# Kernel optimization log

Measured on AMD Instinct MI355X. Metric: run time of the kernel, lower is better.

## Reference

```python
import jax, jax.numpy as jnp
import numpy as np
import math

SEQ_LEN = 32768
DIM = 64
HYPER = [2048, 1024, 512]
POOL = [2, 2]
K = 16
UPDATE_RATE = 0.5
ALPHA = 3.0


def _node_nums():
    n = [SEQ_LEN]
    for p in POOL:
        n.append(n[-1] // p)
    return n[:len(HYPER)]  # [32768, 16384, 8192]


def _init_adj(n, h, k):
    # Faithful port of init_H_indicies for one level: banded 0/1 matrix, then softmax over dim=1
    m = np.zeros((n, h), dtype=np.float32)
    for col in range(h - 1, -1, -1):
        s = max(0, n - k - h + col - 1)
        e = n - h + col
        if s <= e:
            m[s:e + 1, col] = 1.0
    x = m - m.max(axis=1, keepdims=True)
    ex = np.exp(x)
    return (ex / ex.sum(axis=1, keepdims=True)).astype(np.float32)


def setup_inputs() -> dict:
    key = jax.random.key(0)
    ks = jax.random.split(key, 6)
    nn_ = _node_nums()
    inp = {}
    for i, n in enumerate(nn_):
        inp[f"node_emb{i}"] = jax.random.normal(ks[i], (n, DIM), dtype=jnp.float32)
    for i, h in enumerate(HYPER):
        inp[f"edge_emb{i}"] = jax.random.normal(ks[3 + i], (h, DIM), dtype=jnp.float32)
    for i, (n, h) in enumerate(zip(nn_, HYPER)):
        inp[f"adj_init{i}"] = jnp.asarray(_init_adj(n, h, K))
    return inp


def _layer(node, edge, adj_prev):
    # a = node @ edge.T ; cur = softmax(relu(alpha*a), dim=1)
    a = jnp.matmul(node, edge.T)  # [N, E]
    cur = jax.nn.softmax(jax.nn.relu(ALPHA * a), axis=1)
    k = min(cur.shape[1], K)
    _, idx = jax.lax.top_k(cur, k)  # [N, k]
    rows = jnp.arange(cur.shape[0])[:, None]
    mask = jnp.zeros_like(cur).at[rows, idx].set(1.0)  # scatter_ with s1.fill_(1)
    cur = cur * mask
    adj = UPDATE_RATE * cur + (1.0 - UPDATE_RATE) * adj_prev  # EMA blend
    adj = (adj - adj.min()) / (adj.max() - adj.min())  # global minmax norm
    return adj


def _binarize(adj):
    b = (adj > 0.5)
    retain = b.any(axis=0)  # which hyperedges survive compaction (H2index retain_edge)
    return b.astype(jnp.int32), retain


def reference(node_emb0, node_emb1, node_emb2, edge_emb0, edge_emb1, edge_emb2,
              adj_init0, adj_init1, adj_init2):
    nodes = [node_emb0, node_emb1, node_emb2]
    edges = [edge_emb0, edge_emb1, edge_emb2]
    inits = [adj_init0, adj_init1, adj_init2]
    H_list, bins, retains = [], [], []
    for nd, ed, ad in zip(nodes, edges, inits):
        adj = _layer(nd, ed, ad)
        H_list.append(adj)
        b, r = _binarize(adj)
        bins.append(b)
        retains.append(r)
    # Hypergraph fusion (HypergraphFusion is not defined in the source; we use the
    # natural fusion: upsample each coarse level to seq_len resolution by repeating
    # each coarse node over its pooling window, then concat along the hyperedge axis).
    full = []
    factor = 1
    for i, H in enumerate(H_list):
        up = jnp.repeat(H, factor, axis=0)  # [node_num[i]*factor, E_i] == [SEQ_LEN, E_i]
        if up.shape[0] < SEQ_LEN:
            up = jnp.pad(up, ((0, SEQ_LEN - up.shape[0]), (0, 0)))
        full.append(up)
        if i < len(POOL):
            factor *= POOL[i]
    fused_H = jnp.concatenate(full, axis=1)  # [SEQ_LEN, sum(HYPER)]
    fused_bin, fused_retain = _binarize(fused_H)
    return (fused_H, H_list[0], H_list[1], H_list[2],
            bins[0], bins[1], bins[2], fused_bin,
            retains[0], retains[1], retains[2], fused_retain)
```

## Files before the change

### kernel.cpp

```cpp
#include <hip/hip_runtime.h>
#include <cstdint>
#include <cstddef>

#define DIM 64

static constexpr size_t OFF_FH = 0;
static constexpr size_t OFF_H0 = 117440512;
static constexpr size_t OFF_H1 = 184549376;
static constexpr size_t OFF_H2 = 201326592;
static constexpr size_t OFF_B0 = 205520896;
static constexpr size_t OFF_B1 = 272629760;
static constexpr size_t OFF_B2 = 289406976;
static constexpr size_t OFF_FB = 293601280;
static constexpr size_t OFF_R0 = 411041792;
static constexpr size_t OFF_R1 = 411043840;
static constexpr size_t OFF_R2 = 411044864;
static constexpr size_t OFF_RF = 411045376;

__device__ __forceinline__ double exp2split(float x) {
  const float f = x * 1.44269504f;
  const int i = (int)f;
  const float r = f - (float)i;
  const float e = exp2f(r);
  const unsigned long long sc = (unsigned long long)(1023 + i) << 52;
  return (double)e * __longlong_as_double((long long)sc);
}

__device__ __forceinline__ void scan1(float x, int col, unsigned long long* top,
                                      unsigned long long& tmin, double& s) {
  const unsigned long long pk =
      ((unsigned long long)__float_as_uint(x) << 32) |
      (unsigned long long)(0xFFFFFFFFu - (unsigned int)col);
  if (pk > tmin) {
#pragma unroll
    for (int q = 0; q < 16; ++q) top[q] = (top[q] == tmin) ? pk : top[q];
    unsigned long long t2 = top[0];
#pragma unroll
    for (int q = 1; q < 16; ++q) t2 = (top[q] < t2) ? top[q] : t2;
    tmin = t2;
  }
  s += exp2split(x);
}

__global__ void k_init(float* __restrict__ out, unsigned int* __restrict__ wsMM,
                       unsigned long long* __restrict__ wsBlend) {
  const int t = threadIdx.x;
  for (int i = t; i < 7168; i += 256) out[OFF_R0 + i] = 0.0f;
  if (t < 3) {
    wsMM[2 * t + 0] = 0x7F7FFFFFu;
    wsMM[2 * t + 1] = 0u;
    wsBlend[t] = 0ull;
  }
}

__global__ __launch_bounds__(256) void k1(
    const float* __restrict__ node0, const float* __restrict__ node1, const float* __restrict__ node2,
    const float* __restrict__ edge0, const float* __restrict__ edge1, const float* __restrict__ edge2,
    const float* __restrict__ init0, const float* __restrict__ init1, const float* __restrict__ init2,
    int* __restrict__ tIdx0, int* __restrict__ tIdx1, int* __restrict__ tIdx2,
    double* __restrict__ tCur0, double* __restrict__ tCur1, double* __restrict__ tCur2,
    unsigned int* __restrict__ wsMM, unsigned long long* __restrict__ wsBlend) {
  __shared__ float smem[128 * 132];
  __shared__ float sMin[4], sMax[4];
  __shared__ double sBlendW[4];

  const int b = blockIdx.x;
  int lvl, bloc, E;
  const float *node, *edge, *init;
  int* tIdx;
  double* tCur;
  if (b < 256)      { lvl = 0; bloc = b;       node = node0; edge = edge0; init = init0; tIdx = tIdx0; tCur = tCur0; E = 2048; }
  else if (b < 384) { lvl = 1; bloc = b - 256; node = node1; edge = edge1; init = init1; tIdx = tIdx1; tCur = tCur1; E = 1024; }
  else              { lvl = 2; bloc = b - 384; node = node2; edge = edge2; init = init2; tIdx = tIdx2; tCur = tCur2; E = 512;  }

  const int t = threadIdx.x;
  const int lane = t & 63;
  const int wave = t >> 6;
  const int row0 = bloc * 128;
  const int tr8 = (t & 15) << 3;
  const int tc8 = (t >> 4) << 3;
  const int srow = t >> 1;
  const int sl = t & 1;
  float* nB = smem + 64 * 132;

  unsigned long long top[16];
#pragma unroll
  for (int q = 0; q < 16; ++q) top[q] = (unsigned long long)q;
  unsigned long long tmin = 0ull;
  double s0 = 0.0, s1 = 0.0;

  for (int c0 = 0; c0 < E; c0 += 128) {
    __syncthreads();
#pragma unroll
    for (int p = 0; p < 8; ++p) {
      const int idx = t + 256 * p;
      const int r = idx >> 4;
      const int kc = (idx & 15) << 2;
      const float4 v = *(const float4*)(node + (size_t)(row0 + r) * DIM + kc);
      smem[(kc + 0) * 132 + r] = v.x;
      smem[(kc + 1) * 132 + r] = v.y;
      smem[(kc + 2) * 132 + r] = v.z;
      smem[(kc + 3) * 132 + r] = v.w;
      const float4 w = *(const float4*)(edge + (size_t)(c0 + r) * DIM + kc);
      nB[(kc + 0) * 132 + r] = w.x;
      nB[(kc + 1) * 132 + r] = w.y;
      nB[(kc + 2) * 132 + r] = w.z;
      nB[(kc + 3) * 132 + r] = w.w;
    }
    __syncthreads();

    float acc[8][8];
#pragma unroll
    for (int i = 0; i < 8; ++i)
#pragma unroll
      for (int j = 0; j < 8; ++j) acc[i][j] = 0.0f;

#pragma unroll 4
    for (int k = 0; k < 64; ++k) {
      const float4 a0 = *(const float4*)&smem[k * 132 + tr8];
      const float4 a1 = *(const float4*)&smem[k * 132 + tr8 + 4];
      const float4 b0 = *(const float4*)&nB[k * 132 + tc8];
      const float4 b1 = *(const float4*)&nB[k * 132 + tc8 + 4];
      const float av[8] = {a0.x, a0.y, a0.z, a0.w, a1.x, a1.y, a1.z, a1.w};
      const float bv[8] = {b0.x, b0.y, b0.z, b0.w, b1.x, b1.y, b1.z, b1.w};
#pragma unroll
      for (int i = 0; i < 8; ++i)
#pragma unroll
        for (int j = 0; j < 8; ++j) acc[i][j] = fmaf(av[i], bv[j], acc[i][j]);
    }
    __syncthreads();

#pragma unroll
    for (int i = 0; i < 8; ++i) {
      float4 h0, h1;
      h0.x = fmaxf(3.0f * acc[i][0], 0.0f); h0.y = fmaxf(3.0f * acc[i][1], 0.0f);
      h0.z = fmaxf(3.0f * acc[i][2], 0.0f); h0.w = fmaxf(3.0f * acc[i][3], 0.0f);
      h1.x = fmaxf(3.0f * acc[i][4], 0.0f); h1.y = fmaxf(3.0f * acc[i][5], 0.0f);
      h1.z = fmaxf(3.0f * acc[i][6], 0.0f); h1.w = fmaxf(3.0f * acc[i][7], 0.0f);
      *(float4*)&smem[(tr8 + i) * 132 + tc8] = h0;
      *(float4*)&smem[(tr8 + i) * 132 + tc8 + 4] = h1;
    }
    __syncthreads();

#pragma unroll 4
    for (int j = 0; j < 16; ++j) {
      const int cl = (sl << 6) + (j << 2);
      const float4 v = *(const float4*)&smem[srow * 132 + cl];
      const int cb = c0 + cl;
      scan1(v.x, cb + 0, top, tmin, s0);
      scan1(v.y, cb + 1, top, tmin, s1);
      scan1(v.z, cb + 2, top, tmin, s0);
      scan1(v.w, cb + 3, top, tmin, s1);
    }
  }

  unsigned long long win[8];
#pragma unroll 1
  for (int round = 0; round < 16; ++round) {
    unsigned long long lm = top[0];
#pragma unroll
    for (int q = 1; q < 16; ++q) lm = (top[q] > lm) ? top[q] : lm;
    { const unsigned long long o = __shfl_xor(lm, 1); lm = (o > lm) ? o : lm; }
#pragma unroll
    for (int q = 0; q < 16; ++q) top[q] = (top[q] == lm) ? 0ull : top[q];
    if ((round & 1) == sl) win[round >> 1] = lm;
  }

  double sAll = s0 + s1;
  sAll += __shfl_xor(sAll, 1);

  const int grow = row0 + srow;
  const float4* n4 = (const float4*)(node + (size_t)grow * DIM);
  double eh[8];
  int gcv[8];
  double h32sum = 0.0, ehsum = 0.0;
#pragma unroll 1
  for (int w = 0; w < 8; ++w) {
    const float x32 = __uint_as_float((unsigned int)(win[w] >> 32));
    const unsigned int gc = 0xFFFFFFFFu - (unsigned int)(win[w] & 0xFFFFFFFFull);
    const float4* e4 = (const float4*)(edge + (size_t)gc * DIM);
    double acc = 0.0;
#pragma unroll
    for (int j = 0; j < 16; ++j) {
      const float4 a = n4[j], bb = e4[j];
      acc += (double)a.x * (double)bb.x + (double)a.y * (double)bb.y +
             (double)a.z * (double)bb.z + (double)a.w * (double)bb.w;
    }
    const double x64 = fmax(3.0 * acc, 0.0);
    eh[w] = exp(x64);
    ehsum += eh[w];
    h32sum += exp2split(x32);
    gcv[w] = (int)gc;
  }
  h32sum += __shfl_xor(h32sum, 1);
  ehsum += __shfl_xor(ehsum, 1);
  const double sFix = fmax(sAll - h32sum, 0.0) + ehsum;

  double blend = 0.0;
#pragma unroll 1
  for (int w = 0; w < 8; ++w) {
    const double cur = eh[w] / sFix;
    tIdx[(size_t)grow * 16 + 2 * w + sl] = gcv[w];
    tCur[(size_t)grow * 16 + 2 * w + sl] = cur;
    blend = fmax(blend, 0.5 * ((double)init[(size_t)grow * E + gcv[w]] + cur));
  }
#pragma unroll
  for (int d = 1; d < 64; d <<= 1) {
    const double o = __shfl_xor(blend, d);
    blend = fmax(blend, o);
  }
  if (lane == 0) sBlendW[wave] = blend;

  float imn = __uint_as_float(0x7F7FFFFFu), imx = 0.0f;
  const float4* ib = (const float4*)(init + (size_t)row0 * E);
  const int tot = (128 * E) >> 2;
  for (int i = t; i < tot; i += 256) {
    const float4 v = ib[i];
    imn = fminf(imn, fminf(fminf(v.x, v.y), fminf(v.z, v.w)));
    imx = fmaxf(imx, fmaxf(fmaxf(v.x, v.y), fmaxf(v.z, v.w)));
  }
#pragma unroll
  for (int d = 1; d < 64; d <<= 1) {
    imn = fminf(imn, __shfl_xor(imn, d));
    imx = fmaxf(imx, __shfl_xor(imx, d));
  }
  if (lane == 0) { sMin[wave] = imn; sMax[wave] = imx; }
  __syncthreads();
  if (t == 0) {
    const float a = fminf(fminf(sMin[0], sMin[1]), fminf(sMin[2], sMin[3]));
    const float bmx = fmaxf(fmaxf(sMax[0], sMax[1]), fmaxf(sMax[2], sMax[3]));
    atomicMin(wsMM + 2 * lvl + 0, __float_as_uint(a));
    atomicMax(wsMM + 2 * lvl + 1, __float_as_uint(bmx));
    double bl = sBlendW[0];
#pragma unroll
    for (int i = 1; i < 4; ++i) bl = fmax(bl, sBlendW[i]);
    atomicMax(wsBlend + lvl, (unsigned long long)__double_as_longlong(bl));
  }
}

__global__ __launch_bounds__(256) void k2(
    const float* __restrict__ init0, const float* __restrict__ init1, const float* __restrict__ init2,
    const int* __restrict__ tIdx0, const int* __restrict__ tIdx1, const int* __restrict__ tIdx2,
    const double* __restrict__ tCur0, const double* __restrict__ tCur1, const double* __restrict__ tCur2,
    const unsigned int* __restrict__ wsMM, const unsigned long long* __restrict__ wsBlend,
    float* __restrict__ out) {
  __shared__ float fH[3584];
  __shared__ float fB[3584];
  const int r = blockIdx.x;
  const int t = threadIdx.x;
  const int r1 = r >> 1, r2 = r >> 2;

  const double mn0 = 0.5 * (double)__uint_as_float(wsMM[0]);
  const double mx0 = fmax(0.5 * (double)__uint_as_float(wsMM[1]),
                          __longlong_as_double((long long)wsBlend[0]));
  const double inv0 = 1.0 / (mx0 - mn0);
  const double mn1 = 0.5 * (double)__uint_as_float(wsMM[2]);
  const double mx1 = fmax(0.5 * (double)__uint_as_float(wsMM[3]),
                          __longlong_as_double((long long)wsBlend[1]));
  const double inv1 = 1.0 / (mx1 - mn1);
  const double mn2 = 0.5 * (double)__uint_as_float(wsMM[4]);
  const double mx2 = fmax(0.5 * (double)__uint_as_float(wsMM[5]),
                          __longlong_as_double((long long)wsBlend[2]));
  const double inv2 = 1.0 / (mx2 - mn2);

  for (int i = t; i < 896; i += 256) {
    const int c = i << 2;
    float4 v;
    float mnl, il;
    size_t offR, offF;
    if (c < 2048)      { v = *(const float4*)(init0 + (size_t)r  * 2048 + c);
                         mnl = (float)mn0; il = (float)inv0; offR = OFF_R0; offF = (size_t)c; }
    else if (c < 3072) { v = *(const float4*)(init1 + (size_t)r1 * 1024 + (c - 2048));
                         mnl = (float)mn1; il = (float)inv1; offR = OFF_R1 - 2048; offF = (size_t)c; }
    else               { v = *(const float4*)(init2 + (size_t)r2 * 512 + (c - 3072));
                         mnl = (float)mn2; il = (float)inv2; offR = OFF_R2 - 3072; offF = (size_t)c; }
    float4 h, bb;
    h.x = (0.5f * v.x - mnl) * il;
    h.y = (0.5f * v.y - mnl) * il;
    h.z = (0.5f * v.z - mnl) * il;
    h.w = (0.5f * v.w - mnl) * il;
    bb.x = (h.x > 0.5f) ? 1.0f : 0.0f;
    bb.y = (h.y > 0.5f) ? 1.0f : 0.0f;
    bb.z = (h.z > 0.5f) ? 1.0f : 0.0f;
    bb.w = (h.w > 0.5f) ? 1.0f : 0.0f;
    *(float4*)&fH[c] = h;
    *(float4*)&fB[c] = bb;
    if (bb.x + bb.y + bb.z + bb.w > 0.0f) {
      if (bb.x > 0.0f) { out[offR + c + 0] = 1.0f; out[OFF_RF + c + 0] = 1.0f; }
      if (bb.y > 0.0f) { out[offR + c + 1] = 1.0f; out[OFF_RF + c + 1] = 1.0f; }
      if (bb.z > 0.0f) { out[offR + c + 2] = 1.0f; out[OFF_RF + c + 2] = 1.0f; }
      if (bb.w > 0.0f) { out[offR + c + 3] = 1.0f; out[OFF_RF + c + 3] = 1.0f; }
    }
  }
  __syncthreads();

  if (t < 48) {
    const int lv = t >> 4, j = t & 15;
    int rowl, El, off;
    const int* ti; const double* tc; const float* in;
    size_t offR;
    double mnl, il;
    if (lv == 0)      { rowl = r;  El = 2048; off = 0;    ti = tIdx0; tc = tCur0; in = init0; offR = OFF_R0; mnl = mn0; il = inv0; }
    else if (lv == 1) { rowl = r1; El = 1024; off = 2048; ti = tIdx1; tc = tCur1; in = init1; offR = OFF_R1; mnl = mn1; il = inv1; }
    else              { rowl = r2; El = 512;  off = 3072; ti = tIdx2; tc = tCur2; in = init2; offR = OFF_R2; mnl = mn2; il = inv2; }
    const int gc = ti[(size_t)rowl * 16 + j];
    const double cur = tc[(size_t)rowl * 16 + j];
    const double adj = 0.5 * ((double)in[(size_t)rowl * El + gc] + cur);
    const double H = (adj - mnl) * il;
    const float hf = (float)H;
    const float bf = (H > 0.5) ? 1.0f : 0.0f;
    fH[off + gc] = hf;
    fB[off + gc] = bf;
    if (bf > 0.0f) {
      out[offR + gc] = 1.0f;
      out[OFF_RF + off + gc] = 1.0f;
    }
  }
  __syncthreads();

  const float4* sH = (const float4*)fH;
  const float4* sB = (const float4*)fB;
  float4* FH = (float4*)(out + OFF_FH + (size_t)r * 3584);
  float4* FB = (float4*)(out + OFF_FB + (size_t)r * 3584);
  float4* H0 = (float4*)(out + OFF_H0 + (size_t)r * 2048);
  float4* B0 = (float4*)(out + OFF_B0 + (size_t)r * 2048);
  for (int i = t; i < 896; i += 256) { FH[i] = sH[i]; FB[i] = sB[i]; }
  for (int i = t; i < 512; i += 256) { H0[i] = sH[i]; B0[i] = sB[i]; }
  if ((r & 1) == 0) {
    float4* H1 = (float4*)(out + OFF_H1 + (size_t)r1 * 1024);
    float4* B1 = (float4*)(out + OFF_B1 + (size_t)r1 * 1024);
    H1[t] = sH[512 + t];
    B1[t] = sB[512 + t];
  }
  if ((r & 3) == 0 && t < 128) {
    float4* H2 = (float4*)(out + OFF_H2 + (size_t)r2 * 512);
    float4* B2 = (float4*)(out + OFF_B2 + (size_t)r2 * 512);
    H2[t] = sH[768 + t];
    B2[t] = sB[768 + t];
  }
}

extern "C" void kernel_launch(void* const* d_in, const int* in_sizes, int n_in,
                              void* d_out, int out_size, void* d_ws, size_t ws_size,
                              hipStream_t stream) {
  (void)in_sizes; (void)n_in; (void)out_size; (void)ws_size;
  const float* node0 = (const float*)d_in[0];
  const float* node1 = (const float*)d_in[1];
  const float* node2 = (const float*)d_in[2];
  const float* edge0 = (const float*)d_in[3];
  const float* edge1 = (const float*)d_in[4];
  const float* edge2 = (const float*)d_in[5];
  const float* init0 = (const float*)d_in[6];
  const float* init1 = (const float*)d_in[7];
  const float* init2 = (const float*)d_in[8];
  float* out = (float*)d_out;

  unsigned char* ws = (unsigned char*)d_ws;
  unsigned int* wsMM = (unsigned int*)ws;
  unsigned long long* wsBlend = (unsigned long long*)(ws + 32);
  int*    tIdx0 = (int*)(ws + 64);
  int*    tIdx1 = (int*)(ws + 64 + (size_t)(2 << 20));
  int*    tIdx2 = (int*)(ws + 64 + (size_t)(3 << 20));
  double* tCur0 = (double*)(ws + 64 + (size_t)(4 << 20));
  double* tCur1 = (double*)(ws + 64 + (size_t)(8 << 20));
  double* tCur2 = (double*)(ws + 64 + (size_t)(10 << 20));

  k_init<<<1, 256, 0, stream>>>(out, wsMM, wsBlend);
  k1<<<448, 256, 0, stream>>>(node0, node1, node2, edge0, edge1, edge2,
                              init0, init1, init2, tIdx0, tIdx1, tIdx2,
                              tCur0, tCur1, tCur2, wsMM, wsBlend);
  k2<<<32768, 256, 0, stream>>>(init0, init1, init2, tIdx0, tIdx1, tIdx2,
                                tCur0, tCur1, tCur2, wsMM, wsBlend, out);
}
```

Measured before the change: 2.625 ms.

## Split fused GEMM/top-k kernel into GEMM, minmax and per-row wave top-k kernels

The monolithic k1, which ran only 448 blocks, is split in three. k1a computes relu(3*A·Eᵀ) tiles and writes them to a workspace buffer. A separate kmm kernel does the global min/max over the init matrices. k1b assigns one wavefront per row to scan the staged logits, select the top-16 with wave-wide shuffles, and do the fp64 refinement. The aim is to fix poor occupancy and parallelism in the serial per-thread top-k scan, at the cost of writing and re-reading about 450MB of intermediate logits. Nontemporal stores are also added for the k2 output writes.

```diff
diff --git a/kernel.cpp b/kernel.cpp
--- a/kernel.cpp
+++ b/kernel.cpp
@@ -3,6 +3,8 @@
 #include <cstddef>
 
 #define DIM 64
+
+typedef float f32x4 __attribute__((ext_vector_type(4)));
 
 static constexpr size_t OFF_FH = 0;
 static constexpr size_t OFF_H0 = 117440512;
@@ -53,59 +55,39 @@
   }
 }
 
-__global__ __launch_bounds__(256) void k1(
+__global__ __launch_bounds__(256, 2) void k1a(
     const float* __restrict__ node0, const float* __restrict__ node1, const float* __restrict__ node2,
     const float* __restrict__ edge0, const float* __restrict__ edge1, const float* __restrict__ edge2,
-    const float* __restrict__ init0, const float* __restrict__ init1, const float* __restrict__ init2,
-    int* __restrict__ tIdx0, int* __restrict__ tIdx1, int* __restrict__ tIdx2,
-    double* __restrict__ tCur0, double* __restrict__ tCur1, double* __restrict__ tCur2,
-    unsigned int* __restrict__ wsMM, unsigned long long* __restrict__ wsBlend) {
-  __shared__ float smem[128 * 132];
-  __shared__ float sMin[4], sMax[4];
-  __shared__ double sBlendW[4];
+    float* __restrict__ xt0, float* __restrict__ xt1, float* __restrict__ xt2) {
+  __shared__ float sA[64 * 132];
+  __shared__ float sB[64 * 132];
 
   const int b = blockIdx.x;
-  int lvl, bloc, E;
-  const float *node, *edge, *init;
-  int* tIdx;
-  double* tCur;
-  if (b < 256)      { lvl = 0; bloc = b;       node = node0; edge = edge0; init = init0; tIdx = tIdx0; tCur = tCur0; E = 2048; }
-  else if (b < 384) { lvl = 1; bloc = b - 256; node = node1; edge = edge1; init = init1; tIdx = tIdx1; tCur = tCur1; E = 1024; }
-  else              { lvl = 2; bloc = b - 384; node = node2; edge = edge2; init = init2; tIdx = tIdx2; tCur = tCur2; E = 512;  }
+  int bloc, E;
+  const float *node, *edge;
+  float* xt;
+  if (b < 256)      { bloc = b;       node = node0; edge = edge0; xt = xt0; E = 2048; }
+  else if (b < 384) { bloc = b - 256; node = node1; edge = edge1; xt = xt1; E = 1024; }
+  else              { bloc = b - 384; node = node2; edge = edge2; xt = xt2; E = 512;  }
 
   const int t = threadIdx.x;
-  const int lane = t & 63;
-  const int wave = t >> 6;
   const int row0 = bloc * 128;
-  const int tr8 = (t & 15) << 3;
-  const int tc8 = (t >> 4) << 3;
-  const int srow = t >> 1;
-  const int sl = t & 1;
-  float* nB = smem + 64 * 132;
-
-  unsigned long long top[16];
-#pragma unroll
-  for (int q = 0; q < 16; ++q) top[q] = (unsigned long long)q;
-  unsigned long long tmin = 0ull;
-  double s0 = 0.0, s1 = 0.0;
+  const int tr8 = (t >> 4) << 3;
+  const int tc8 = (t & 15) << 3;
 
   for (int c0 = 0; c0 < E; c0 += 128) {
     __syncthreads();
 #pragma unroll
     for (int p = 0; p < 8; ++p) {
-      const int idx = t + 256 * p;
-      const int r = idx >> 4;
-      const int kc = (idx & 15) << 2;
+      const int idx = t + (p << 8);
+      const int kc = (idx >> 7) << 2;
+      const int r = idx & 127;
       const float4 v = *(const float4*)(node + (size_t)(row0 + r) * DIM + kc);
-      smem[(kc + 0) * 132 + r] = v.x;
-      smem[(kc + 1) * 132 + r] = v.y;
-      smem[(kc + 2) * 132 + r] = v.z;
-      smem[(kc + 3) * 132 + r] = v.w;
+      sA[(kc + 0) * 132 + r] = v.x; sA[(kc + 1) * 132 + r] = v.y;
+      sA[(kc + 2) * 132 + r] = v.z; sA[(kc + 3) * 132 + r] = v.w;
       const float4 w = *(const float4*)(edge + (size_t)(c0 + r) * DIM + kc);
-      nB[(kc + 0) * 132 + r] = w.x;
-      nB[(kc + 1) * 132 + r] = w.y;
-      nB[(kc + 2) * 132 + r] = w.z;
-      nB[(kc + 3) * 132 + r] = w.w;
+      sB[(kc + 0) * 132 + r] = w.x; sB[(kc + 1) * 132 + r] = w.y;
+      sB[(kc + 2) * 132 + r] = w.z; sB[(kc + 3) * 132 + r] = w.w;
     }
     __syncthreads();
 
@@ -115,12 +97,12 @@
 #pragma unroll
       for (int j = 0; j < 8; ++j) acc[i][j] = 0.0f;
 
-#pragma unroll 4
+#pragma unroll 2
     for (int k = 0; k < 64; ++k) {
-      const float4 a0 = *(const float4*)&smem[k * 132 + tr8];
-      const float4 a1 = *(const float4*)&smem[k * 132 + tr8 + 4];
-      const float4 b0 = *(const float4*)&nB[k * 132 + tc8];
-      const float4 b1 = *(const float4*)&nB[k * 132 + tc8 + 4];
+      const float4 a0 = *(const float4*)&sA[k * 132 + tr8];
+      const float4 a1 = *(const float4*)&sA[k * 132 + tr8 + 4];
+      const float4 b0 = *(const float4*)&sB[k * 132 + tc8];
+      const float4 b1 = *(const float4*)&sB[k * 132 + tc8 + 4];
       const float av[8] = {a0.x, a0.y, a0.z, a0.w, a1.x, a1.y, a1.z, a1.w};
       const float bv[8] = {b0.x, b0.y, b0.z, b0.w, b1.x, b1.y, b1.z, b1.w};
 #pragma unroll
@@ -128,56 +110,119 @@
 #pragma unroll
         for (int j = 0; j < 8; ++j) acc[i][j] = fmaf(av[i], bv[j], acc[i][j]);
     }
-    __syncthreads();
 
 #pragma unroll
     for (int i = 0; i < 8; ++i) {
-      float4 h0, h1;
+      f32x4 h0, h1;
       h0.x = fmaxf(3.0f * acc[i][0], 0.0f); h0.y = fmaxf(3.0f * acc[i][1], 0.0f);
       h0.z = fmaxf(3.0f * acc[i][2], 0.0f); h0.w = fmaxf(3.0f * acc[i][3], 0.0f);
       h1.x = fmaxf(3.0f * acc[i][4], 0.0f); h1.y = fmaxf(3.0f * acc[i][5], 0.0f);
       h1.z = fmaxf(3.0f * acc[i][6], 0.0f); h1.w = fmaxf(3.0f * acc[i][7], 0.0f);
-      *(float4*)&smem[(tr8 + i) * 132 + tc8] = h0;
-      *(float4*)&smem[(tr8 + i) * 132 + tc8 + 4] = h1;
-    }
-    __syncthreads();
-
-#pragma unroll 4
-    for (int j = 0; j < 16; ++j) {
-      const int cl = (sl << 6) + (j << 2);
-      const float4 v = *(const float4*)&smem[srow * 132 + cl];
-      const int cb = c0 + cl;
-      scan1(v.x, cb + 0, top, tmin, s0);
-      scan1(v.y, cb + 1, top, tmin, s1);
-      scan1(v.z, cb + 2, top, tmin, s0);
-      scan1(v.w, cb + 3, top, tmin, s1);
-    }
-  }
-
-  unsigned long long win[8];
+      float* dst = xt + (size_t)(row0 + tr8 + i) * E + c0 + tc8;
+      *(f32x4*)dst = h0;
+      *(f32x4*)(dst + 4) = h1;
+    }
+  }
+}
+
+__global__ __launch_bounds__(256) void kmm(
+    const float* __restrict__ init0, const float* __restrict__ init1,
+    const float* __restrict__ init2, unsigned int* __restrict__ wsMM) {
+  __shared__ float sMin[3][4], sMax[3][4];
+  const int t = threadIdx.x;
+  const int lane = t & 63;
+  const int wave = t >> 6;
+  const int gid = blockIdx.x * 256 + t;
+  const int stride = gridDim.x * 256;
+  const float* inits[3] = {init0, init1, init2};
+  const int n4[3] = {16777216, 4194304, 1048576};
+#pragma unroll
+  for (int lv = 0; lv < 3; ++lv) {
+    float mn = __uint_as_float(0x7F7FFFFFu), mx = 0.0f;
+    const float4* p = (const float4*)inits[lv];
+    for (int i = gid; i < n4[lv]; i += stride) {
+      const float4 v = p[i];
+      mn = fminf(mn, fminf(fminf(v.x, v.y), fminf(v.z, v.w)));
+      mx = fmaxf(mx, fmaxf(fmaxf(v.x, v.y), fmaxf(v.z, v.w)));
+    }
+#pragma unroll
+    for (int d = 1; d < 64; d <<= 1) {
+      mn = fminf(mn, __shfl_xor(mn, d));
+      mx = fmaxf(mx, __shfl_xor(mx, d));
+    }
+    if (lane == 0) { sMin[lv][wave] = mn; sMax[lv][wave] = mx; }
+  }
+  __syncthreads();
+  if (t < 3) {
+    const float a = fminf(fminf(sMin[t][0], sMin[t][1]), fminf(sMin[t][2], sMin[t][3]));
+    const float b = fmaxf(fmaxf(sMax[t][0], sMax[t][1]), fmaxf(sMax[t][2], sMax[t][3]));
+    atomicMin(wsMM + 2 * t + 0, __float_as_uint(a));
+    atomicMax(wsMM + 2 * t + 1, __float_as_uint(b));
+  }
+}
+
+__global__ __launch_bounds__(256) void k1b(
+    const float* __restrict__ node0, const float* __restrict__ node1, const float* __restrict__ node2,
+    const float* __restrict__ edge0, const float* __restrict__ edge1, const float* __restrict__ edge2,
+    const float* __restrict__ init0, const float* __restrict__ init1, const float* __restrict__ init2,
+    const float* __restrict__ xt0, const float* __restrict__ xt1, const float* __restrict__ xt2,
+    int* __restrict__ tIdx0, int* __restrict__ tIdx1, int* __restrict__ tIdx2,
+    double* __restrict__ tCur0, double* __restrict__ tCur1, double* __restrict__ tCur2,
+    unsigned long long* __restrict__ wsBlend) {
+  __shared__ double sBlend[4];
+  const int t = threadIdx.x;
+  const int lane = t & 63;
+  const int gw = blockIdx.x * 4 + (t >> 6);
+  int lvl, row, E;
+  const float *xt, *node, *edge, *init;
+  int* tIdx;
+  double* tCur;
+  if (gw < 32768)      { lvl = 0; row = gw;          E = 2048; xt = xt0; node = node0; edge = edge0; init = init0; tIdx = tIdx0; tCur = tCur0; }
+  else if (gw < 49152) { lvl = 1; row = gw - 32768;  E = 1024; xt = xt1; node = node1; edge = edge1; init = init1; tIdx = tIdx1; tCur = tCur1; }
+  else                 { lvl = 2; row = gw - 49152;  E = 512;  xt = xt2; node = node2; edge = edge2; init = init2; tIdx = tIdx2; tCur = tCur2; }
+
+  const float* xrow = xt + (size_t)row * E;
+  unsigned long long top[16];
+#pragma unroll
+  for (int q = 0; q < 16; ++q) top[q] = (unsigned long long)q;
+  unsigned long long tmin = 0ull;
+  double s = 0.0;
+  const int nIt = E >> 8;
+  for (int j = 0; j < nIt; ++j) {
+    const int c4 = (lane + (j << 6)) << 2;
+    const float4 v = *(const float4*)(xrow + c4);
+    scan1(v.x, c4 + 0, top, tmin, s);
+    scan1(v.y, c4 + 1, top, tmin, s);
+    scan1(v.z, c4 + 2, top, tmin, s);
+    scan1(v.w, c4 + 3, top, tmin, s);
+  }
+
+  unsigned long long mywin = 0ull;
 #pragma unroll 1
   for (int round = 0; round < 16; ++round) {
     unsigned long long lm = top[0];
 #pragma unroll
     for (int q = 1; q < 16; ++q) lm = (top[q] > lm) ? top[q] : lm;
-    { const unsigned long long o = __shfl_xor(lm, 1); lm = (o > lm) ? o : lm; }
+#pragma unroll
+    for (int d = 1; d < 64; d <<= 1) {
+      const unsigned long long o = __shfl_xor(lm, d);
+      lm = (o > lm) ? o : lm;
+    }
 #pragma unroll
     for (int q = 0; q < 16; ++q) top[q] = (top[q] == lm) ? 0ull : top[q];
-    if ((round & 1) == sl) win[round >> 1] = lm;
-  }
-
-  double sAll = s0 + s1;
-  sAll += __shfl_xor(sAll, 1);
-
-  const int grow = row0 + srow;
-  const float4* n4 = (const float4*)(node + (size_t)grow * DIM);
-  double eh[8];
-  int gcv[8];
-  double h32sum = 0.0, ehsum = 0.0;
-#pragma unroll 1
-  for (int w = 0; w < 8; ++w) {
-    const float x32 = __uint_as_float((unsigned int)(win[w] >> 32));
-    const unsigned int gc = 0xFFFFFFFFu - (unsigned int)(win[w] & 0xFFFFFFFFull);
+    if (lane == round) mywin = lm;
+  }
+
+  double sAll = s;
+#pragma unroll
+  for (int d = 1; d < 64; d <<= 1) sAll += __shfl_xor(sAll, d);
+
+  double eh = 0.0, h32 = 0.0;
+  int gc = 0;
+  if (lane < 16) {
+    const float x32 = __uint_as_float((unsigned int)(mywin >> 32));
+    gc = (int)(0xFFFFFFFFu - (unsigned int)(mywin & 0xFFFFFFFFull));
+    const float4* n4 = (const float4*)(node + (size_t)row * DIM);
     const float4* e4 = (const float4*)(edge + (size_t)gc * DIM);
     double acc = 0.0;
 #pragma unroll
@@ -186,54 +231,35 @@
       acc += (double)a.x * (double)bb.x + (double)a.y * (double)bb.y +
              (double)a.z * (double)bb.z + (double)a.w * (double)bb.w;
     }
-    const double x64 = fmax(3.0 * acc, 0.0);
-    eh[w] = exp(x64);
-    ehsum += eh[w];
-    h32sum += exp2split(x32);
-    gcv[w] = (int)gc;
-  }
-  h32sum += __shfl_xor(h32sum, 1);
-  ehsum += __shfl_xor(ehsum, 1);
+    eh = exp(fmax(3.0 * acc, 0.0));
+    h32 = exp2split(x32);
+  }
+  double ehsum = eh, h32sum = h32;
+#pragma unroll
+  for (int d = 1; d < 64; d <<= 1) {
+    ehsum += __shfl_xor(ehsum, d);
+    h32sum += __shfl_xor(h32sum, d);
+  }
   const double sFix = fmax(sAll - h32sum, 0.0) + ehsum;
 
   double blend = 0.0;
-#pragma unroll 1
-  for (int w = 0; w < 8; ++w) {
-    const double cur = eh[w] / sFix;
-    tIdx[(size_t)grow * 16 + 2 * w + sl] = gcv[w];
-    tCur[(size_t)grow * 16 + 2 * w + sl] = cur;
-    blend = fmax(blend, 0.5 * ((double)init[(size_t)grow * E + gcv[w]] + cur));
+  if (lane < 16) {
+    const double cur = eh / sFix;
+    tIdx[(size_t)row * 16 + lane] = gc;
+    tCur[(size_t)row * 16 + lane] = cur;
+    blend = 0.5 * ((double)init[(size_t)row * E + gc] + cur);
   }
 #pragma unroll
   for (int d = 1; d < 64; d <<= 1) {
     const double o = __shfl_xor(blend, d);
     blend = fmax(blend, o);
   }
-  if (lane == 0) sBlendW[wave] = blend;
-
-  float imn = __uint_as_float(0x7F7FFFFFu), imx = 0.0f;
-  const float4* ib = (const float4*)(init + (size_t)row0 * E);
-  const int tot = (128 * E) >> 2;
-  for (int i = t; i < tot; i += 256) {
-    const float4 v = ib[i];
-    imn = fminf(imn, fminf(fminf(v.x, v.y), fminf(v.z, v.w)));
-    imx = fmaxf(imx, fmaxf(fmaxf(v.x, v.y), fmaxf(v.z, v.w)));
-  }
-#pragma unroll
-  for (int d = 1; d < 64; d <<= 1) {
-    imn = fminf(imn, __shfl_xor(imn, d));
-    imx = fmaxf(imx, __shfl_xor(imx, d));
-  }
-  if (lane == 0) { sMin[wave] = imn; sMax[wave] = imx; }
+  if (lane == 0) sBlend[t >> 6] = blend;
   __syncthreads();
   if (t == 0) {
-    const float a = fminf(fminf(sMin[0], sMin[1]), fminf(sMin[2], sMin[3]));
-    const float bmx = fmaxf(fmaxf(sMax[0], sMax[1]), fmaxf(sMax[2], sMax[3]));
-    atomicMin(wsMM + 2 * lvl + 0, __float_as_uint(a));
-    atomicMax(wsMM + 2 * lvl + 1, __float_as_uint(bmx));
-    double bl = sBlendW[0];
-#pragma unroll
-    for (int i = 1; i < 4; ++i) bl = fmax(bl, sBlendW[i]);
+    double bl = sBlend[0];
+#pragma unroll
+    for (int i = 1; i < 4; ++i) bl = fmax(bl, sBlend[i]);
     atomicMax(wsBlend + lvl, (unsigned long long)__double_as_longlong(bl));
   }
 }
@@ -267,13 +293,13 @@
     const int c = i << 2;
     float4 v;
     float mnl, il;
-    size_t offR, offF;
+    size_t offR;
     if (c < 2048)      { v = *(const float4*)(init0 + (size_t)r  * 2048 + c);
-                         mnl = (float)mn0; il = (float)inv0; offR = OFF_R0; offF = (size_t)c; }
+                         mnl = (float)mn0; il = (float)inv0; offR = OFF_R0; }
     else if (c < 3072) { v = *(const float4*)(init1 + (size_t)r1 * 1024 + (c - 2048));
-                         mnl = (float)mn1; il = (float)inv1; offR = OFF_R1 - 2048; offF = (size_t)c; }
+                         mnl = (float)mn1; il = (float)inv1; offR = OFF_R1 - 2048; }
     else               { v = *(const float4*)(init2 + (size_t)r2 * 512 + (c - 3072));
-                         mnl = (float)mn2; il = (float)inv2; offR = OFF_R2 - 3072; offF = (size_t)c; }
+                         mnl = (float)mn2; il = (float)inv2; offR = OFF_R2 - 3072; }
     float4 h, bb;
     h.x = (0.5f * v.x - mnl) * il;
     h.y = (0.5f * v.y - mnl) * il;
@@ -318,25 +344,31 @@
   }
   __syncthreads();
 
-  const float4* sH = (const float4*)fH;
-  const float4* sB = (const float4*)fB;
-  float4* FH = (float4*)(out + OFF_FH + (size_t)r * 3584);
-  float4* FB = (float4*)(out + OFF_FB + (size_t)r * 3584);
-  float4* H0 = (float4*)(out + OFF_H0 + (size_t)r * 2048);
-  float4* B0 = (float4*)(out + OFF_B0 + (size_t)r * 2048);
-  for (int i = t; i < 896; i += 256) { FH[i] = sH[i]; FB[i] = sB[i]; }
-  for (int i = t; i < 512; i += 256) { H0[i] = sH[i]; B0[i] = sB[i]; }
+  const f32x4* sH = (const f32x4*)fH;
+  const f32x4* sB = (const f32x4*)fB;
+  f32x4* FH = (f32x4*)(out + OFF_FH + (size_t)r * 3584);
+  f32x4* FB = (f32x4*)(out + OFF_FB + (size_t)r * 3584);
+  f32x4* H0 = (f32x4*)(out + OFF_H0 + (size_t)r * 2048);
+  f32x4* B0 = (f32x4*)(out + OFF_B0 + (size_t)r * 2048);
+  for (int i = t; i < 896; i += 256) {
+    __builtin_nontemporal_store(sH[i], &FH[i]);
+    __builtin_nontemporal_store(sB[i], &FB[i]);
+  }
+  for (int i = t; i < 512; i += 256) {
+    __builtin_nontemporal_store(sH[i], &H0[i]);
+    __builtin_nontemporal_store(sB[i], &B0[i]);
+  }
   if ((r & 1) == 0) {
-    float4* H1 = (float4*)(out + OFF_H1 + (size_t)r1 * 1024);
-    float4* B1 = (float4*)(out + OFF_B1 + (size_t)r1 * 1024);
-    H1[t] = sH[512 + t];
-    B1[t] = sB[512 + t];
+    f32x4* H1 = (f32x4*)(out + OFF_H1 + (size_t)r1 * 1024);
+    f32x4* B1 = (f32x4*)(out + OFF_B1 + (size_t)r1 * 1024);
+    __builtin_nontemporal_store(sH[512 + t], &H1[t]);
+    __builtin_nontemporal_store(sB[512 + t], &B1[t]);
   }
   if ((r & 3) == 0 && t < 128) {
-    float4* H2 = (float4*)(out + OFF_H2 + (size_t)r2 * 512);
-    float4* B2 = (float4*)(out + OFF_B2 + (size_t)r2 * 512);
-    H2[t] = sH[768 + t];
-    B2[t] = sB[768 + t];
+    f32x4* H2 = (f32x4*)(out + OFF_H2 + (size_t)r2 * 512);
+    f32x4* B2 = (f32x4*)(out + OFF_B2 + (size_t)r2 * 512);
+    __builtin_nontemporal_store(sH[768 + t], &H2[t]);
+    __builtin_nontemporal_store(sB[768 + t], &B2[t]);
   }
 }
 
@@ -358,17 +390,22 @@
   unsigned char* ws = (unsigned char*)d_ws;
   unsigned int* wsMM = (unsigned int*)ws;
   unsigned long long* wsBlend = (unsigned long long*)(ws + 32);
-  int*    tIdx0 = (int*)(ws + 64);
-  int*    tIdx1 = (int*)(ws + 64 + (size_t)(2 << 20));
-  int*    tIdx2 = (int*)(ws + 64 + (size_t)(3 << 20));
-  double* tCur0 = (double*)(ws + 64 + (size_t)(4 << 20));
-  double* tCur1 = (double*)(ws + 64 + (size_t)(8 << 20));
-  double* tCur2 = (double*)(ws + 64 + (size_t)(10 << 20));
+  int*    tIdx0 = (int*)(ws + (size_t)(1 << 20));
+  int*    tIdx1 = (int*)(ws + (size_t)(3 << 20));
+  int*    tIdx2 = (int*)(ws + (size_t)(4 << 20));
+  double* tCur0 = (double*)(ws + (size_t)(5 << 20));
+  double* tCur1 = (double*)(ws + (size_t)(9 << 20));
+  double* tCur2 = (double*)(ws + (size_t)(11 << 20));
+  float*  xt0   = (float*)(ws + (size_t)(16 << 20));
+  float*  xt1   = (float*)(ws + (size_t)(288 << 20));
+  float*  xt2   = (float*)(ws + (size_t)(356 << 20));
 
   k_init<<<1, 256, 0, stream>>>(out, wsMM, wsBlend);
-  k1<<<448, 256, 0, stream>>>(node0, node1, node2, edge0, edge1, edge2,
-                              init0, init1, init2, tIdx0, tIdx1, tIdx2,
-                              tCur0, tCur1, tCur2, wsMM, wsBlend);
+  k1a<<<448, 256, 0, stream>>>(node0, node1, node2, edge0, edge1, edge2, xt0, xt1, xt2);
+  kmm<<<1024, 256, 0, stream>>>(init0, init1, init2, wsMM);
+  k1b<<<14336, 256, 0, stream>>>(node0, node1, node2, edge0, edge1, edge2,
+                                 init0, init1, init2, xt0, xt1, xt2,
+                                 tIdx0, tIdx1, tIdx2, tCur0, tCur1, tCur2, wsBlend);
   k2<<<32768, 256, 0, stream>>>(init0, init1, init2, tIdx0, tIdx1, tIdx2,
                                 tCur0, tCur1, tCur2, wsMM, wsBlend, out);
 }
```

Result: no change. 2.631 ms (+0.3%).
